# Optimization experiments

Hardware: AMD Instinct MI355X
Metric: run time of the kernel (lower is better)

## Reference

```python
import jax, jax.numpy as jnp
import numpy as np

N, IN_DIM, H_DIM, POS_DIM, K, M, E, OUT_DIM = 50000, 256, 96, 32, 64, 128, 800000, 40
HID = H_DIM + POS_DIM  # 128

def _lin(key, fan_out, fan_in):
    k1, k2 = jax.random.split(key)
    bnd = 1.0 / np.sqrt(fan_in)
    W = jax.random.uniform(k1, (fan_out, fan_in), minval=-bnd, maxval=bnd, dtype=jnp.float32)
    b = jax.random.uniform(k2, (fan_out,), minval=-bnd, maxval=bnd, dtype=jnp.float32)
    return W, b

def setup_inputs() -> dict:
    key = jax.random.key(0)
    ks = jax.random.split(key, 12)
    x = jax.random.normal(ks[0], (N, IN_DIM), dtype=jnp.float32)
    eigenvectors = jax.random.normal(ks[1], (N, M), dtype=jnp.float32)
    eigenvalues = jax.random.uniform(ks[2], (M,), dtype=jnp.float32)
    edge_index = jax.random.randint(ks[3], (2, E), 0, N, dtype=jnp.int64)
    W_feat, b_feat = _lin(ks[4], H_DIM, IN_DIM)
    alpha = jax.random.uniform(ks[5], (K, POS_DIM), minval=-1/np.sqrt(K), maxval=1/np.sqrt(K), dtype=jnp.float32)
    Wl1, bl1 = _lin(ks[6], HID, HID)
    Wr1, _ = _lin(ks[7], HID, HID)
    Wl2, bl2 = _lin(ks[8], HID, HID)
    Wr2, _ = _lin(ks[9], HID, HID)
    W_ro, b_ro = _lin(ks[10], OUT_DIM, HID)
    return dict(x=x, eigenvectors=eigenvectors, eigenvalues=eigenvalues, edge_index=edge_index,
                W_feat=W_feat, b_feat=b_feat, alpha=alpha,
                Wl1=Wl1, bl1=bl1, Wr1=Wr1, Wl2=Wl2, bl2=bl2, Wr2=Wr2,
                W_ro=W_ro, b_ro=b_ro)

def _sage_conv(x, src, dst, Wl, bl, Wr):
    # PyG SAGEConv (mean aggr): out = lin_l(mean_{j->i} x_j) + lin_r(x_i)
    n = x.shape[0]
    agg = jax.ops.segment_sum(x[src], dst, num_segments=n)           # [N, HID]
    cnt = jax.ops.segment_sum(jnp.ones_like(dst, dtype=x.dtype), dst, num_segments=n)
    mean = agg / jnp.maximum(cnt, 1.0)[:, None]
    return mean @ Wl.T + bl + x @ Wr.T

def reference(x, eigenvectors, eigenvalues, edge_index,
              W_feat, b_feat, alpha, Wl1, bl1, Wr1, Wl2, bl2, Wr2, W_ro, b_ro):
    # normalize eigenvectors per column to [-1, 1]
    ev_min = jnp.min(eigenvectors, axis=0, keepdims=True)
    ev_max = jnp.max(eigenvectors, axis=0, keepdims=True)
    ev = (eigenvectors - ev_min) / (ev_max - ev_min) * 2.0 - 1.0
    # normalize eigenvalues to [-1, 1], Chebyshev basis via arccos/cos
    lmin, lmax = jnp.min(eigenvalues), jnp.max(eigenvalues)
    lam = (eigenvalues - lmin) / (lmax - lmin) * 2.0 - 1.0
    theta = jnp.arccos(lam)[:, None] * jnp.arange(K, dtype=lam.dtype)[None, :]  # [M, K]
    pe = jnp.cos(theta) @ alpha                                                  # [M, pos_dim]
    pos = ev @ pe                                                                # [N, pos_dim]
    h = jnp.concatenate([x @ W_feat.T + b_feat, pos], axis=-1)                   # [N, HID]
    src, dst = edge_index[0], edge_index[1]
    h = jax.nn.relu(_sage_conv(h, src, dst, Wl1, bl1, Wr1))
    h = jax.nn.relu(_sage_conv(h, src, dst, Wl2, bl2, Wr2))
    out = jax.nn.log_softmax(h @ W_ro.T + b_ro, axis=-1)
    return out, pe
```

## Files before the change

### kernel.cpp

```cpp
#include <hip/hip_runtime.h>
#include <math.h>

#define N        50000
#define IN_DIM   256
#define H_DIM    96
#define POS_DIM  32
#define KCH      64
#define M        128
#define NE       800000
#define OUT_DIM  40
#define HID      128
#define NSCAN    196
#define NTILES   ((N + 63) / 64)
#define NBK      391
#define BKCAP    2560
#define NSCATB   512
#define SREG     1563

typedef __attribute__((ext_vector_type(8))) short short8v;
typedef __attribute__((ext_vector_type(4))) float float4v;

__device__ __forceinline__ unsigned short f2bf(float f){
  unsigned u = __float_as_uint(f);
  u += 0x7fffu + ((u >> 16) & 1u);
  return (unsigned short)(u >> 16);
}
__device__ __forceinline__ float bf_lo(unsigned u){ return __uint_as_float(u << 16); }
__device__ __forceinline__ float bf_hi(unsigned u){ return __uint_as_float(u & 0xffff0000u); }

__device__ __forceinline__ unsigned enc_key(float f){
  unsigned u = __float_as_uint(f);
  return (u & 0x80000000u) ? ~u : (u | 0x80000000u);
}
__device__ __forceinline__ float dec_key(unsigned k){
  unsigned u = (k & 0x80000000u) ? (k ^ 0x80000000u) : ~k;
  return __uint_as_float(u);
}

__global__ void k_init(unsigned* __restrict__ encmn, unsigned* __restrict__ encmx,
                       short* __restrict__ WT_pos, float* __restrict__ bias_pos,
                       int* __restrict__ bkt_cnt){
  int i = blockIdx.x*blockDim.x + threadIdx.x;
  if (i < M){ encmn[i] = 0xFFFFFFFFu; encmx[i] = 0u; bias_pos[i] = 0.f; }
  if (i < M*M) WT_pos[i] = 0;
  if (i < NBK) bkt_cnt[i] = 0;
}

__global__ __launch_bounds__(256) void k_colminmax(const float* __restrict__ ev,
    unsigned* __restrict__ encmn, unsigned* __restrict__ encmx){
  __shared__ float4 smn[256], smx[256];
  int tid = threadIdx.x;
  int cg  = tid & 31;
  int rs  = blockIdx.x*8 + (tid >> 5);
  int stride = gridDim.x*8;
  float4 mn = make_float4( 3.4e38f,  3.4e38f,  3.4e38f,  3.4e38f);
  float4 mx = make_float4(-3.4e38f, -3.4e38f, -3.4e38f, -3.4e38f);
  #pragma unroll 4
  for (int r = rs; r < N; r += stride){
    float4 v = *(const float4*)&ev[(size_t)r*M + cg*4];
    mn.x = fminf(mn.x, v.x); mn.y = fminf(mn.y, v.y);
    mn.z = fminf(mn.z, v.z); mn.w = fminf(mn.w, v.w);
    mx.x = fmaxf(mx.x, v.x); mx.y = fmaxf(mx.y, v.y);
    mx.z = fmaxf(mx.z, v.z); mx.w = fmaxf(mx.w, v.w);
  }
  smn[tid] = mn; smx[tid] = mx;
  __syncthreads();
  for (int s = 128; s >= 32; s >>= 1){
    if (tid < s){
      float4 a = smn[tid], b = smn[tid + s];
      smn[tid] = make_float4(fminf(a.x,b.x), fminf(a.y,b.y), fminf(a.z,b.z), fminf(a.w,b.w));
      float4 c = smx[tid], d = smx[tid + s];
      smx[tid] = make_float4(fmaxf(c.x,d.x), fmaxf(c.y,d.y), fmaxf(c.z,d.z), fmaxf(c.w,d.w));
    }
    __syncthreads();
  }
  if (tid < 32){
    float4 a = smn[tid], b = smx[tid];
    atomicMin(&encmn[tid*4+0], enc_key(a.x));
    atomicMin(&encmn[tid*4+1], enc_key(a.y));
    atomicMin(&encmn[tid*4+2], enc_key(a.z));
    atomicMin(&encmn[tid*4+3], enc_key(a.w));
    atomicMax(&encmx[tid*4+0], enc_key(b.x));
    atomicMax(&encmx[tid*4+1], enc_key(b.y));
    atomicMax(&encmx[tid*4+2], enc_key(b.z));
    atomicMax(&encmx[tid*4+3], enc_key(b.w));
  }
}

__global__ __launch_bounds__(128) void k_eig_minmax(const float* __restrict__ eigval,
                                                    float* __restrict__ lmm){
  __shared__ float red[M];
  int t = threadIdx.x;
  float v = eigval[t];
  red[t] = v; __syncthreads();
  for (int s = 64; s; s >>= 1){ if (t < s) red[t] = fminf(red[t], red[t+s]); __syncthreads(); }
  if (t == 0) lmm[0] = red[0];
  __syncthreads();
  red[t] = v; __syncthreads();
  for (int s = 64; s; s >>= 1){ if (t < s) red[t] = fmaxf(red[t], red[t+s]); __syncthreads(); }
  if (t == 0) lmm[1] = red[0];
}

__global__ __launch_bounds__(256) void k_pe(
    const float* __restrict__ eigval, const float* __restrict__ alpha,
    const unsigned* __restrict__ encmn, const unsigned* __restrict__ encmx,
    const float* __restrict__ lmm,
    short* __restrict__ WT_pos, float* __restrict__ pe_raw,
    float* __restrict__ pe_out){
  int g = blockIdx.x*256 + threadIdx.x;
  int m = g >> 5, p = g & 31;
  float lmin = lmm[0], lmax = lmm[1];
  float v = eigval[m];
  float lam = (v - lmin)/(lmax - lmin)*2.0f - 1.0f;
  lam = fminf(1.0f, fmaxf(-1.0f, lam));
  float t0 = 1.0f, t1 = lam;
  float acc = alpha[p] + lam*alpha[POS_DIM + p];
  float two_lam = lam + lam;
  #pragma unroll
  for (int k = 2; k < KCH; ++k){
    float t2 = fmaf(two_lam, t1, -t0);
    acc = fmaf(t2, alpha[k*POS_DIM + p], acc);
    t0 = t1; t1 = t2;
  }
  pe_out[g] = acc;
  pe_raw[g] = acc;
  float cmn = dec_key(encmn[m]);
  float cmx = dec_key(encmx[m]);
  float A = 2.0f/(cmx - cmn);
  WT_pos[p*M + m] = (short)f2bf(A*acc);
}

__global__ __launch_bounds__(256) void k_bias(
    const unsigned* __restrict__ encmn, const unsigned* __restrict__ encmx,
    const float* __restrict__ pe_raw, float* __restrict__ bias_pos){
  __shared__ float s[256];
  int tid = threadIdx.x;
  int p = tid >> 3, c = tid & 7;
  float sum = 0.f;
  for (int m = c*16; m < c*16 + 16; ++m){
    float cmn = dec_key(encmn[m]);
    float cmx = dec_key(encmx[m]);
    float A = 2.0f/(cmx - cmn);
    float B = -cmn*A - 1.0f;
    sum += B*pe_raw[m*POS_DIM + p];
  }
  s[tid] = sum;
  __syncthreads();
  if (c == 0){
    float t = 0.f;
    #pragma unroll
    for (int j = 0; j < 8; ++j) t += s[p*8 + j];
    bias_pos[p] = t;
  }
}

__global__ void k_prep_w(const float* __restrict__ Wf, const float* __restrict__ bfeat,
                         const float* __restrict__ Wl1, const float* __restrict__ Wr1,
                         const float* __restrict__ Wl2, const float* __restrict__ Wr2,
                         const float* __restrict__ Wro, const float* __restrict__ bro,
                         short* __restrict__ WTf, float* __restrict__ biasf,
                         short* __restrict__ Wc1, short* __restrict__ Wc2,
                         short* __restrict__ WTro, float* __restrict__ biasro){
  int i = blockIdx.x*256 + threadIdx.x;
  if (i < 128*256){
    int c = i >> 8, k = i & 255;
    WTf[i] = (c < H_DIM) ? (short)f2bf(Wf[c*IN_DIM + k]) : (short)0;
    Wc1[i] = (short)f2bf((k < HID) ? Wl1[c*HID + k] : Wr1[c*HID + k - HID]);
    Wc2[i] = (short)f2bf((k < HID) ? Wl2[c*HID + k] : Wr2[c*HID + k - HID]);
  }
  if (i < 48*128){
    int c = i >> 7, k = i & 127;
    WTro[i] = (c < OUT_DIM) ? (short)f2bf(Wro[c*HID + k]) : (short)0;
  }
  if (i < 128) biasf[i] = (i < H_DIM) ? bfeat[i] : 0.f;
  if (i >= 128 && i < 176) biasro[i - 128] = (i - 128 < OUT_DIM) ? bro[i - 128] : 0.f;
}

template<int KD, bool TWOSRC, bool RELU>
__global__ __launch_bounds__(256) void k_gemm(
    const void* __restrict__ A0v, const void* __restrict__ A1v,
    const short* __restrict__ WT, const float* __restrict__ bias,
    unsigned short* __restrict__ outp, int c_used)
{
  constexpr int KSTEPS = KD/32;
  constexpr int CHR    = KD/8;
  __shared__ short a_lds[64*KD];

  int tid = threadIdx.x;
  int wid = tid >> 6, lane = tid & 63;
  int colBase = wid*32;
  int lrow = lane & 15, lk = (lane >> 4)*8;

  short8v bfrag[KSTEPS][2];
  #pragma unroll
  for (int s = 0; s < KSTEPS; ++s)
    #pragma unroll
    for (int ct = 0; ct < 2; ++ct){
      int col = colBase + ct*16 + lrow;
      bfrag[s][ct] = *(const short8v*)&WT[col*KD + s*32 + lk];
    }
  float b0 = bias[colBase + lrow], b1 = bias[colBase + 16 + lrow];

  for (int tile = blockIdx.x; tile < NTILES; tile += gridDim.x){
    int n0 = tile*64;
    __syncthreads();
    #pragma unroll
    for (int c = tid; c < 64*CHR; c += 256){
      int row = c / CHR;
      int k8  = c % CHR;
      int gn  = min(n0 + row, N-1);
      short8v vv;
      if constexpr (TWOSRC){
        const short* src = (k8 < 16) ? ((const short*)A0v + (size_t)gn*HID + k8*8)
                                     : ((const short*)A1v + (size_t)gn*HID + (k8-16)*8);
        vv = *(const short8v*)src;
      } else {
        const float* src = (const float*)A0v + (size_t)gn*KD + k8*8;
        float4v f0 = *(const float4v*)src;
        float4v f1 = *(const float4v*)(src + 4);
        vv[0] = (short)f2bf(f0[0]); vv[1] = (short)f2bf(f0[1]);
        vv[2] = (short)f2bf(f0[2]); vv[3] = (short)f2bf(f0[3]);
        vv[4] = (short)f2bf(f1[0]); vv[5] = (short)f2bf(f1[1]);
        vv[6] = (short)f2bf(f1[2]); vv[7] = (short)f2bf(f1[3]);
      }
      unsigned off = (unsigned)(row*(KD*2) + k8*16);
      off ^= (unsigned)((row & 7) << 4);
      *(short8v*)((char*)a_lds + off) = vv;
    }
    __syncthreads();
    float4v acc[4][2];
    #pragma unroll
    for (int nt = 0; nt < 4; ++nt){
      acc[nt][0] = (float4v){0.f,0.f,0.f,0.f};
      acc[nt][1] = (float4v){0.f,0.f,0.f,0.f};
    }
    #pragma unroll
    for (int s = 0; s < KSTEPS; ++s){
      #pragma unroll
      for (int nt = 0; nt < 4; ++nt){
        int row = nt*16 + lrow;
        unsigned off = (unsigned)(row*(KD*2) + (s*32 + lk)*2);
        off ^= (unsigned)((row & 7) << 4);
        short8v a = *(const short8v*)((const char*)a_lds + off);
        acc[nt][0] = __builtin_amdgcn_mfma_f32_16x16x32_bf16(a, bfrag[s][0], acc[nt][0], 0, 0, 0);
        acc[nt][1] = __builtin_amdgcn_mfma_f32_16x16x32_bf16(a, bfrag[s][1], acc[nt][1], 0, 0, 0);
      }
    }
    if (colBase < c_used){
      int rbase = (lane >> 4)*4;
      #pragma unroll
      for (int nt = 0; nt < 4; ++nt){
        #pragma unroll
        for (int ct = 0; ct < 2; ++ct){
          int col = colBase + ct*16 + lrow;
          float bb = ct ? b1 : b0;
          #pragma unroll
          for (int r = 0; r < 4; ++r){
            int node = n0 + nt*16 + rbase + r;
            if (node < N){
              float v = acc[nt][ct][r] + bb;
              if (RELU) v = fmaxf(v, 0.f);
              outp[(size_t)node*HID + col] = f2bf(v);
            }
          }
        }
      }
    }
  }
}

__global__ __launch_bounds__(256) void k_hist(const int* __restrict__ dst,
                                              int* __restrict__ bkt_cnt){
  __shared__ int h[NBK];
  int tid = threadIdx.x;
  for (int i = tid; i < NBK; i += 256) h[i] = 0;
  __syncthreads();
  for (int e = blockIdx.x*256 + tid; e < NE; e += gridDim.x*256)
    atomicAdd(&h[dst[e] >> 7], 1);
  __syncthreads();
  for (int i = tid; i < NBK; i += 256){
    int c = h[i];
    if (c) atomicAdd(&bkt_cnt[i], c);
  }
}

__global__ __launch_bounds__(512) void k_bktscan(const int* __restrict__ bkt_cnt,
    int* __restrict__ bkt_start, int* __restrict__ bkt_cursor){
  __shared__ int s[512];
  int t = threadIdx.x;
  int v = (t < NBK) ? bkt_cnt[t] : 0;
  s[t] = v;
  __syncthreads();
  for (int st = 1; st < 512; st <<= 1){
    int a = (t >= st) ? s[t-st] : 0;
    __syncthreads();
    s[t] += a;
    __syncthreads();
  }
  int excl = s[t] - v;
  if (t < NBK){ bkt_start[t] = excl; bkt_cursor[t] = excl; }
  if (t == 0) bkt_start[NBK] = NE;
}

__global__ __launch_bounds__(256) void k_bscatter(const int* __restrict__ src,
    const int* __restrict__ dst, int* __restrict__ bkt_cursor,
    unsigned* __restrict__ estage){
  __shared__ int lcnt[NBK];
  __shared__ int lbase[NBK];
  int tid = threadIdx.x;
  int e0 = blockIdx.x*SREG;
  int e1 = min(e0 + SREG, NE);
  for (int i = tid; i < NBK; i += 256) lcnt[i] = 0;
  __syncthreads();
  for (int e = e0 + tid; e < e1; e += 256)
    atomicAdd(&lcnt[dst[e] >> 7], 1);
  __syncthreads();
  for (int i = tid; i < NBK; i += 256){
    int c = lcnt[i];
    lbase[i] = c ? atomicAdd(&bkt_cursor[i], c) : 0;
    lcnt[i] = 0;
  }
  __syncthreads();
  for (int e = e0 + tid; e < e1; e += 256){
    int d = dst[e];
    int b = d >> 7;
    int slot = lbase[b] + atomicAdd(&lcnt[b], 1);
    estage[slot] = (unsigned)src[e] | ((unsigned)(d & 127) << 16);
  }
}

__global__ __launch_bounds__(256) void k_bcsr(const int* __restrict__ bkt_start,
    const unsigned* __restrict__ estage, unsigned short* __restrict__ csr,
    int* __restrict__ row_ptr){
  __shared__ unsigned eb[BKCAP];
  __shared__ int ncnt[128], sc[128], noff[128];
  int tid = threadIdx.x;
  int b = blockIdx.x;
  int s = bkt_start[b], e = bkt_start[b+1];
  int cnt = min(e - s, BKCAP);
  for (int i = tid; i < cnt; i += 256) eb[i] = estage[s + i];
  if (tid < 128) ncnt[tid] = 0;
  __syncthreads();
  for (int i = tid; i < cnt; i += 256)
    atomicAdd(&ncnt[(eb[i] >> 16) & 127], 1);
  __syncthreads();
  if (tid < 128) sc[tid] = ncnt[tid];
  __syncthreads();
  for (int st = 1; st < 128; st <<= 1){
    int a = (tid < 128 && tid >= st) ? sc[tid-st] : 0;
    __syncthreads();
    if (tid < 128) sc[tid] += a;
    __syncthreads();
  }
  if (tid < 128){
    int excl = sc[tid] - ncnt[tid];
    noff[tid] = excl;
    int node = b*128 + tid;
    if (node <= N) row_ptr[node] = s + excl;
    ncnt[tid] = 0;
  }
  __syncthreads();
  for (int i = tid; i < cnt; i += 256){
    unsigned v = eb[i];
    int ld = (v >> 16) & 127;
    int slot = noff[ld] + atomicAdd(&ncnt[ld], 1);
    csr[s + slot] = (unsigned short)(v & 0xffffu);
  }
}

__global__ __launch_bounds__(256) void k_agg_b(const unsigned* __restrict__ h,
    const int* __restrict__ row_ptr, const unsigned short* __restrict__ csr,
    unsigned* __restrict__ outm){
  int gid = blockIdx.x*blockDim.x + threadIdx.x;
  int i = gid >> 6;
  int lane = gid & 63;
  if (i >= N) return;
  int grp = lane >> 4;
  int lc  = lane & 15;
  int b = row_ptr[i], e = row_ptr[i+1];
  float a[8] = {0.f,0.f,0.f,0.f,0.f,0.f,0.f,0.f};
  for (int j = b + grp; j < e; j += 4){
    int s = csr[j];
    uint4 v = *(const uint4*)&h[(size_t)s*64 + lc*4];
    a[0] += bf_lo(v.x); a[1] += bf_hi(v.x);
    a[2] += bf_lo(v.y); a[3] += bf_hi(v.y);
    a[4] += bf_lo(v.z); a[5] += bf_hi(v.z);
    a[6] += bf_lo(v.w); a[7] += bf_hi(v.w);
  }
  #pragma unroll
  for (int k = 0; k < 8; ++k){
    a[k] += __shfl_xor(a[k], 16, 64);
    a[k] += __shfl_xor(a[k], 32, 64);
  }
  if (grp == 0){
    float inv = 1.0f / fmaxf((float)(e - b), 1.0f);
    uint4 o;
    o.x = (unsigned)f2bf(a[0]*inv) | ((unsigned)f2bf(a[1]*inv) << 16);
    o.y = (unsigned)f2bf(a[2]*inv) | ((unsigned)f2bf(a[3]*inv) << 16);
    o.z = (unsigned)f2bf(a[4]*inv) | ((unsigned)f2bf(a[5]*inv) << 16);
    o.w = (unsigned)f2bf(a[6]*inv) | ((unsigned)f2bf(a[7]*inv) << 16);
    *(uint4*)&outm[(size_t)i*64 + lc*4] = o;
  }
}

__global__ __launch_bounds__(256) void k_readout(const short* __restrict__ hb,
    const short* __restrict__ WTro, const float* __restrict__ biasro,
    float* __restrict__ out){
  __shared__ short a_lds[64*HID];
  int tid = threadIdx.x;
  int wid = tid >> 6, lane = tid & 63;
  int lrow = lane & 15, lk = (lane >> 4)*8;

  short8v bfrag[4][3];
  #pragma unroll
  for (int s = 0; s < 4; ++s)
    #pragma unroll
    for (int t = 0; t < 3; ++t){
      int col = t*16 + lrow;
      bfrag[s][t] = *(const short8v*)&WTro[col*HID + s*32 + lk];
    }
  float bias[3] = { biasro[lrow], biasro[16 + lrow], biasro[32 + lrow] };
  bool val2 = lrow < 8;

  for (int tile = blockIdx.x; tile < NTILES; tile += gridDim.x){
    int n0 = tile*64;
    __syncthreads();
    #pragma unroll
    for (int c = tid; c < 64*16; c += 256){
      int row = c >> 4, k8 = c & 15;
      int gn = min(n0 + row, N-1);
      short8v vv = *(const short8v*)(hb + (size_t)gn*HID + k8*8);
      unsigned off = (unsigned)(row*256 + k8*16);
      off ^= (unsigned)((row & 7) << 4);
      *(short8v*)((char*)a_lds + off) = vv;
    }
    __syncthreads();
    float4v acc[3];
    acc[0] = (float4v){0.f,0.f,0.f,0.f};
    acc[1] = (float4v){0.f,0.f,0.f,0.f};
    acc[2] = (float4v){0.f,0.f,0.f,0.f};
    #pragma unroll
    for (int s = 0; s < 4; ++s){
      int row = wid*16 + lrow;
      unsigned off = (unsigned)(row*256 + (s*32 + lk)*2);
      off ^= (unsigned)((row & 7) << 4);
      short8v a = *(const short8v*)((const char*)a_lds + off);
      acc[0] = __builtin_amdgcn_mfma_f32_16x16x32_bf16(a, bfrag[s][0], acc[0], 0, 0, 0);
      acc[1] = __builtin_amdgcn_mfma_f32_16x16x32_bf16(a, bfrag[s][1], acc[1], 0, 0, 0);
      acc[2] = __builtin_amdgcn_mfma_f32_16x16x32_bf16(a, bfrag[s][2], acc[2], 0, 0, 0);
    }
    #pragma unroll
    for (int r = 0; r < 4; ++r){
      float v0 = acc[0][r] + bias[0];
      float v1 = acc[1][r] + bias[1];
      float v2 = acc[2][r] + bias[2];
      float m = fmaxf(v0, v1);
      m = fmaxf(m, val2 ? v2 : -3.4e38f);
      #pragma unroll
      for (int off = 1; off < 16; off <<= 1) m = fmaxf(m, __shfl_xor(m, off, 64));
      float e = expf(v0 - m) + expf(v1 - m) + (val2 ? expf(v2 - m) : 0.f);
      #pragma unroll
      for (int off = 1; off < 16; off <<= 1) e += __shfl_xor(e, off, 64);
      float lz = m + logf(e);
      int node = n0 + wid*16 + (lane >> 4)*4 + r;
      if (node < N){
        out[(size_t)node*OUT_DIM + lrow]      = v0 - lz;
        out[(size_t)node*OUT_DIM + 16 + lrow] = v1 - lz;
        if (val2) out[(size_t)node*OUT_DIM + 32 + lrow] = v2 - lz;
      }
    }
  }
}

extern "C" void kernel_launch(void* const* d_in, const int* in_sizes, int n_in,
                              void* d_out, int out_size, void* d_ws, size_t ws_size,
                              hipStream_t stream){
  const float* x     = (const float*)d_in[0];
  const float* ev    = (const float*)d_in[1];
  const float* eigv  = (const float*)d_in[2];
  const int*   ei    = (const int*)d_in[3];
  const float* Wf    = (const float*)d_in[4];
  const float* bf    = (const float*)d_in[5];
  const float* alpha = (const float*)d_in[6];
  const float* Wl1   = (const float*)d_in[7];
  const float* bl1   = (const float*)d_in[8];
  const float* Wr1   = (const float*)d_in[9];
  const float* Wl2   = (const float*)d_in[10];
  const float* bl2   = (const float*)d_in[11];
  const float* Wr2   = (const float*)d_in[12];
  const float* Wro   = (const float*)d_in[13];
  const float* bro   = (const float*)d_in[14];
  float* out = (float*)d_out;

  short* h0b    = (short*)d_ws;
  short* h1b    = h0b + (size_t)N*HID;
  short* meanb  = h1b + (size_t)N*HID;
  short* WTf    = meanb + (size_t)N*HID;
  short* Wc1    = WTf + 128*256;
  short* Wc2    = Wc1 + 128*256;
  short* WT_pos = Wc2 + 128*256;
  short* WTro   = WT_pos + 128*128;
  float* biasf    = (float*)(WTro + 48*128);
  float* bias_pos = biasf + 128;
  float* biasro   = bias_pos + 128;
  unsigned* encmn = (unsigned*)(biasro + 48);
  unsigned* encmx = encmn + M;
  int* bkt_cnt    = (int*)(encmx + M);
  int* bkt_start  = bkt_cnt + NBK;
  int* bkt_cursor = bkt_start + NBK + 1;
  int* row_ptr    = bkt_cursor + NBK;
  unsigned* estage = (unsigned*)(row_ptr + N + 1);
  unsigned short* csr = (unsigned short*)(estage + NE);
  float* pe_raw = (float*)(csr + NE);
  float* lmm    = pe_raw + M*POS_DIM;

  const int* srcA = ei;
  const int* dstA = ei + NE;

  k_init<<<NSCAN, 256, 0, stream>>>(encmn, encmx, WT_pos, bias_pos, bkt_cnt);
  k_colminmax<<<256, 256, 0, stream>>>(ev, encmn, encmx);
  k_eig_minmax<<<1, 128, 0, stream>>>(eigv, lmm);
  k_pe<<<16, 256, 0, stream>>>(eigv, alpha, encmn, encmx, lmm, WT_pos, pe_raw,
                               out + (size_t)N*OUT_DIM);
  k_bias<<<1, 256, 0, stream>>>(encmn, encmx, pe_raw, bias_pos);
  k_prep_w<<<128, 256, 0, stream>>>(Wf, bf, Wl1, Wr1, Wl2, Wr2, Wro, bro,
                                    WTf, biasf, Wc1, Wc2, WTro, biasro);
  k_hist<<<512, 256, 0, stream>>>(dstA, bkt_cnt);
  k_bktscan<<<1, 512, 0, stream>>>(bkt_cnt, bkt_start, bkt_cursor);
  k_bscatter<<<NSCATB, 256, 0, stream>>>(srcA, dstA, bkt_cursor, estage);
  k_bcsr<<<NBK, 256, 0, stream>>>(bkt_start, estage, csr, row_ptr);
  k_gemm<256,false,false><<<NTILES, 256, 0, stream>>>(x, nullptr, WTf, biasf,
      (unsigned short*)h0b, 128);
  k_gemm<128,false,false><<<NTILES, 256, 0, stream>>>(ev, nullptr, WT_pos, bias_pos,
      (unsigned short*)(h0b + H_DIM), 32);
  k_agg_b<<<(N*64)/256, 256, 0, stream>>>((const unsigned*)h0b, row_ptr, csr, (unsigned*)meanb);
  k_gemm<256,true,true><<<NTILES, 256, 0, stream>>>(meanb, h0b, Wc1, bl1,
      (unsigned short*)h1b, 128);
  k_agg_b<<<(N*64)/256, 256, 0, stream>>>((const unsigned*)h1b, row_ptr, csr, (unsigned*)meanb);
  k_gemm<256,true,true><<<NTILES, 256, 0, stream>>>(meanb, h1b, Wc2, bl2,
      (unsigned short*)h0b, 128);
  k_readout<<<NTILES, 256, 0, stream>>>(h0b, WTro, biasro, out);
}
```

Before: 235.2 us.

## Fuse input GEMMs, conv2 with readout, eig minmax into PE, unroll aggregation

Merges the feature and positional-encoding GEMMs into one kernel that stages x and eigenvectors together in LDS, with the fourth wave handling the positional columns. Fuses the second SAGE conv GEMM with the readout and log-softmax through an LDS buffer, so the intermediate hidden state is never written to or re-read from global memory. Folds the eigenvalue min/max reduction into the PE kernel and unrolls the neighbor aggregation loop by two to keep more loads in flight. This removes three launches and several global round trips, at the cost of a larger LDS footprint (48KB plus 16KB per block) and an imbalanced wave in the input GEMM.

```diff
diff --git a/kernel.cpp b/kernel.cpp
--- a/kernel.cpp
+++ b/kernel.cpp
@@ -87,29 +87,22 @@
   }
 }
 
-__global__ __launch_bounds__(128) void k_eig_minmax(const float* __restrict__ eigval,
-                                                    float* __restrict__ lmm){
-  __shared__ float red[M];
-  int t = threadIdx.x;
-  float v = eigval[t];
-  red[t] = v; __syncthreads();
-  for (int s = 64; s; s >>= 1){ if (t < s) red[t] = fminf(red[t], red[t+s]); __syncthreads(); }
-  if (t == 0) lmm[0] = red[0];
-  __syncthreads();
-  red[t] = v; __syncthreads();
-  for (int s = 64; s; s >>= 1){ if (t < s) red[t] = fmaxf(red[t], red[t+s]); __syncthreads(); }
-  if (t == 0) lmm[1] = red[0];
-}
-
 __global__ __launch_bounds__(256) void k_pe(
     const float* __restrict__ eigval, const float* __restrict__ alpha,
     const unsigned* __restrict__ encmn, const unsigned* __restrict__ encmx,
-    const float* __restrict__ lmm,
     short* __restrict__ WT_pos, float* __restrict__ pe_raw,
     float* __restrict__ pe_out){
-  int g = blockIdx.x*256 + threadIdx.x;
+  __shared__ float rmn[128], rmx[128];
+  int tid = threadIdx.x;
+  if (tid < 128){ float v = eigval[tid]; rmn[tid] = v; rmx[tid] = v; }
+  __syncthreads();
+  for (int s = 64; s; s >>= 1){
+    if (tid < s){ rmn[tid] = fminf(rmn[tid], rmn[tid+s]); rmx[tid] = fmaxf(rmx[tid], rmx[tid+s]); }
+    __syncthreads();
+  }
+  float lmin = rmn[0], lmax = rmx[0];
+  int g = blockIdx.x*256 + tid;
   int m = g >> 5, p = g & 31;
-  float lmin = lmm[0], lmax = lmm[1];
   float v = eigval[m];
   float lam = (v - lmin)/(lmax - lmin)*2.0f - 1.0f;
   lam = fminf(1.0f, fmaxf(-1.0f, lam));
@@ -176,28 +169,125 @@
   if (i >= 128 && i < 176) biasro[i - 128] = (i - 128 < OUT_DIM) ? bro[i - 128] : 0.f;
 }
 
-template<int KD, bool TWOSRC, bool RELU>
-__global__ __launch_bounds__(256) void k_gemm(
-    const void* __restrict__ A0v, const void* __restrict__ A1v,
+__global__ __launch_bounds__(256) void k_gemm_in(
+    const float* __restrict__ x, const float* __restrict__ ev,
+    const short* __restrict__ WTf, const float* __restrict__ biasf,
+    const short* __restrict__ WT_pos, const float* __restrict__ bias_pos,
+    unsigned short* __restrict__ outp)
+{
+  __shared__ short a_lds[64*384];
+  int tid = threadIdx.x;
+  int wid = tid >> 6, lane = tid & 63;
+  int lrow = lane & 15, lk = (lane >> 4)*8;
+  bool isPos = (wid == 3);
+
+  short8v bfragF[8][2];
+  short8v bfragP[4][2];
+  float b0, b1;
+  if (!isPos){
+    int colBase = wid*32;
+    #pragma unroll
+    for (int s = 0; s < 8; ++s)
+      #pragma unroll
+      for (int ct = 0; ct < 2; ++ct){
+        int col = colBase + ct*16 + lrow;
+        bfragF[s][ct] = *(const short8v*)&WTf[col*256 + s*32 + lk];
+      }
+    b0 = biasf[colBase + lrow]; b1 = biasf[colBase + 16 + lrow];
+  } else {
+    #pragma unroll
+    for (int s = 0; s < 4; ++s)
+      #pragma unroll
+      for (int ct = 0; ct < 2; ++ct){
+        int col = ct*16 + lrow;
+        bfragP[s][ct] = *(const short8v*)&WT_pos[col*128 + s*32 + lk];
+      }
+    b0 = bias_pos[lrow]; b1 = bias_pos[16 + lrow];
+  }
+
+  for (int tile = blockIdx.x; tile < NTILES; tile += gridDim.x){
+    int n0 = tile*64;
+    __syncthreads();
+    for (int c = tid; c < 64*48; c += 256){
+      int row = c / 48, k8 = c % 48;
+      int gn = min(n0 + row, N-1);
+      const float* src = (k8 < 32) ? &x[(size_t)gn*IN_DIM + k8*8]
+                                   : &ev[(size_t)gn*M + (k8-32)*8];
+      float4v f0 = *(const float4v*)src;
+      float4v f1 = *(const float4v*)(src + 4);
+      short8v vv;
+      vv[0] = (short)f2bf(f0[0]); vv[1] = (short)f2bf(f0[1]);
+      vv[2] = (short)f2bf(f0[2]); vv[3] = (short)f2bf(f0[3]);
+      vv[4] = (short)f2bf(f1[0]); vv[5] = (short)f2bf(f1[1]);
+      vv[6] = (short)f2bf(f1[2]); vv[7] = (short)f2bf(f1[3]);
+      unsigned off = (unsigned)(row*768 + k8*16) ^ (unsigned)((row & 7) << 4);
+      *(short8v*)((char*)a_lds + off) = vv;
+    }
+    __syncthreads();
+    float4v acc[4][2];
+    #pragma unroll
+    for (int nt = 0; nt < 4; ++nt){
+      acc[nt][0] = (float4v){0.f,0.f,0.f,0.f};
+      acc[nt][1] = (float4v){0.f,0.f,0.f,0.f};
+    }
+    if (!isPos){
+      #pragma unroll
+      for (int s = 0; s < 8; ++s)
+        #pragma unroll
+        for (int nt = 0; nt < 4; ++nt){
+          int row = nt*16 + lrow;
+          unsigned off = (unsigned)(row*768 + (s*32 + lk)*2) ^ (unsigned)((row & 7) << 4);
+          short8v a = *(const short8v*)((const char*)a_lds + off);
+          acc[nt][0] = __builtin_amdgcn_mfma_f32_16x16x32_bf16(a, bfragF[s][0], acc[nt][0], 0, 0, 0);
+          acc[nt][1] = __builtin_amdgcn_mfma_f32_16x16x32_bf16(a, bfragF[s][1], acc[nt][1], 0, 0, 0);
+        }
+    } else {
+      #pragma unroll
+      for (int s = 0; s < 4; ++s)
+        #pragma unroll
+        for (int nt = 0; nt < 4; ++nt){
+          int row = nt*16 + lrow;
+          unsigned off = (unsigned)(row*768 + 512 + (s*32 + lk)*2) ^ (unsigned)((row & 7) << 4);
+          short8v a = *(const short8v*)((const char*)a_lds + off);
+          acc[nt][0] = __builtin_amdgcn_mfma_f32_16x16x32_bf16(a, bfragP[s][0], acc[nt][0], 0, 0, 0);
+          acc[nt][1] = __builtin_amdgcn_mfma_f32_16x16x32_bf16(a, bfragP[s][1], acc[nt][1], 0, 0, 0);
+        }
+    }
+    int colBase = isPos ? 96 : wid*32;
+    int rbase = (lane >> 4)*4;
+    #pragma unroll
+    for (int nt = 0; nt < 4; ++nt)
+      #pragma unroll
+      for (int ct = 0; ct < 2; ++ct){
+        int col = colBase + ct*16 + lrow;
+        float bb = ct ? b1 : b0;
+        #pragma unroll
+        for (int r = 0; r < 4; ++r){
+          int node = n0 + nt*16 + rbase + r;
+          if (node < N) outp[(size_t)node*HID + col] = f2bf(acc[nt][ct][r] + bb);
+        }
+      }
+  }
+}
+
+__global__ __launch_bounds__(256) void k_conv(
+    const short* __restrict__ A0, const short* __restrict__ A1,
     const short* __restrict__ WT, const float* __restrict__ bias,
-    unsigned short* __restrict__ outp, int c_used)
+    unsigned short* __restrict__ outp)
 {
-  constexpr int KSTEPS = KD/32;
-  constexpr int CHR    = KD/8;
-  __shared__ short a_lds[64*KD];
-
+  __shared__ short a_lds[64*256];
   int tid = threadIdx.x;
   int wid = tid >> 6, lane = tid & 63;
   int colBase = wid*32;
   int lrow = lane & 15, lk = (lane >> 4)*8;
 
-  short8v bfrag[KSTEPS][2];
+  short8v bfrag[8][2];
   #pragma unroll
-  for (int s = 0; s < KSTEPS; ++s)
+  for (int s = 0; s < 8; ++s)
     #pragma unroll
     for (int ct = 0; ct < 2; ++ct){
       int col = colBase + ct*16 + lrow;
-      bfrag[s][ct] = *(const short8v*)&WT[col*KD + s*32 + lk];
+      bfrag[s][ct] = *(const short8v*)&WT[col*256 + s*32 + lk];
     }
   float b0 = bias[colBase + lrow], b1 = bias[colBase + 16 + lrow];
 
@@ -205,26 +295,13 @@
     int n0 = tile*64;
     __syncthreads();
     #pragma unroll
-    for (int c = tid; c < 64*CHR; c += 256){
-      int row = c / CHR;
-      int k8  = c % CHR;
-      int gn  = min(n0 + row, N-1);
-      short8v vv;
-      if constexpr (TWOSRC){
-        const short* src = (k8 < 16) ? ((const short*)A0v + (size_t)gn*HID + k8*8)
-                                     : ((const short*)A1v + (size_t)gn*HID + (k8-16)*8);
-        vv = *(const short8v*)src;
-      } else {
-        const float* src = (const float*)A0v + (size_t)gn*KD + k8*8;
-        float4v f0 = *(const float4v*)src;
-        float4v f1 = *(const float4v*)(src + 4);
-        vv[0] = (short)f2bf(f0[0]); vv[1] = (short)f2bf(f0[1]);
-        vv[2] = (short)f2bf(f0[2]); vv[3] = (short)f2bf(f0[3]);
-        vv[4] = (short)f2bf(f1[0]); vv[5] = (short)f2bf(f1[1]);
-        vv[6] = (short)f2bf(f1[2]); vv[7] = (short)f2bf(f1[3]);
-      }
-      unsigned off = (unsigned)(row*(KD*2) + k8*16);
-      off ^= (unsigned)((row & 7) << 4);
+    for (int c = tid; c < 64*32; c += 256){
+      int row = c >> 5, k8 = c & 31;
+      int gn = min(n0 + row, N-1);
+      const short* src = (k8 < 16) ? (A0 + (size_t)gn*HID + k8*8)
+                                   : (A1 + (size_t)gn*HID + (k8-16)*8);
+      short8v vv = *(const short8v*)src;
+      unsigned off = (unsigned)(row*512 + k8*16) ^ (unsigned)((row & 7) << 4);
       *(short8v*)((char*)a_lds + off) = vv;
     }
     __syncthreads();
@@ -235,35 +312,143 @@
       acc[nt][1] = (float4v){0.f,0.f,0.f,0.f};
     }
     #pragma unroll
-    for (int s = 0; s < KSTEPS; ++s){
+    for (int s = 0; s < 8; ++s)
       #pragma unroll
       for (int nt = 0; nt < 4; ++nt){
         int row = nt*16 + lrow;
-        unsigned off = (unsigned)(row*(KD*2) + (s*32 + lk)*2);
-        off ^= (unsigned)((row & 7) << 4);
+        unsigned off = (unsigned)(row*512 + (s*32 + lk)*2) ^ (unsigned)((row & 7) << 4);
         short8v a = *(const short8v*)((const char*)a_lds + off);
         acc[nt][0] = __builtin_amdgcn_mfma_f32_16x16x32_bf16(a, bfrag[s][0], acc[nt][0], 0, 0, 0);
         acc[nt][1] = __builtin_amdgcn_mfma_f32_16x16x32_bf16(a, bfrag[s][1], acc[nt][1], 0, 0, 0);
       }
-    }
-    if (colBase < c_used){
-      int rbase = (lane >> 4)*4;
+    int rbase = (lane >> 4)*4;
+    #pragma unroll
+    for (int nt = 0; nt < 4; ++nt)
+      #pragma unroll
+      for (int ct = 0; ct < 2; ++ct){
+        int col = colBase + ct*16 + lrow;
+        float bb = ct ? b1 : b0;
+        #pragma unroll
+        for (int r = 0; r < 4; ++r){
+          int node = n0 + nt*16 + rbase + r;
+          if (node < N)
+            outp[(size_t)node*HID + col] = f2bf(fmaxf(acc[nt][ct][r] + bb, 0.f));
+        }
+      }
+  }
+}
+
+__global__ __launch_bounds__(256) void k_conv_ro(
+    const short* __restrict__ A0, const short* __restrict__ A1,
+    const short* __restrict__ WT, const float* __restrict__ bias,
+    const short* __restrict__ WTro, const float* __restrict__ biasro,
+    float* __restrict__ out)
+{
+  __shared__ short a_lds[64*256];
+  __shared__ short o_lds[64*128];
+  int tid = threadIdx.x;
+  int wid = tid >> 6, lane = tid & 63;
+  int colBase = wid*32;
+  int lrow = lane & 15, lk = (lane >> 4)*8;
+
+  short8v bfrag[8][2];
+  #pragma unroll
+  for (int s = 0; s < 8; ++s)
+    #pragma unroll
+    for (int ct = 0; ct < 2; ++ct){
+      int col = colBase + ct*16 + lrow;
+      bfrag[s][ct] = *(const short8v*)&WT[col*256 + s*32 + lk];
+    }
+  float b0 = bias[colBase + lrow], b1 = bias[colBase + 16 + lrow];
+
+  short8v bfragR[4][3];
+  #pragma unroll
+  for (int s = 0; s < 4; ++s)
+    #pragma unroll
+    for (int t = 0; t < 3; ++t){
+      int col = t*16 + lrow;
+      bfragR[s][t] = *(const short8v*)&WTro[col*HID + s*32 + lk];
+    }
+  float biasR[3] = { biasro[lrow], biasro[16 + lrow], biasro[32 + lrow] };
+  bool val2 = lrow < 8;
+
+  for (int tile = blockIdx.x; tile < NTILES; tile += gridDim.x){
+    int n0 = tile*64;
+    __syncthreads();
+    #pragma unroll
+    for (int c = tid; c < 64*32; c += 256){
+      int row = c >> 5, k8 = c & 31;
+      int gn = min(n0 + row, N-1);
+      const short* src = (k8 < 16) ? (A0 + (size_t)gn*HID + k8*8)
+                                   : (A1 + (size_t)gn*HID + (k8-16)*8);
+      short8v vv = *(const short8v*)src;
+      unsigned off = (unsigned)(row*512 + k8*16) ^ (unsigned)((row & 7) << 4);
+      *(short8v*)((char*)a_lds + off) = vv;
+    }
+    __syncthreads();
+    float4v acc[4][2];
+    #pragma unroll
+    for (int nt = 0; nt < 4; ++nt){
+      acc[nt][0] = (float4v){0.f,0.f,0.f,0.f};
+      acc[nt][1] = (float4v){0.f,0.f,0.f,0.f};
+    }
+    #pragma unroll
+    for (int s = 0; s < 8; ++s)
       #pragma unroll
       for (int nt = 0; nt < 4; ++nt){
+        int row = nt*16 + lrow;
+        unsigned off = (unsigned)(row*512 + (s*32 + lk)*2) ^ (unsigned)((row & 7) << 4);
+        short8v a = *(const short8v*)((const char*)a_lds + off);
+        acc[nt][0] = __builtin_amdgcn_mfma_f32_16x16x32_bf16(a, bfrag[s][0], acc[nt][0], 0, 0, 0);
+        acc[nt][1] = __builtin_amdgcn_mfma_f32_16x16x32_bf16(a, bfrag[s][1], acc[nt][1], 0, 0, 0);
+      }
+    int rbase = (lane >> 4)*4;
+    #pragma unroll
+    for (int nt = 0; nt < 4; ++nt)
+      #pragma unroll
+      for (int ct = 0; ct < 2; ++ct){
+        int col = colBase + ct*16 + lrow;
+        float bb = ct ? b1 : b0;
         #pragma unroll
-        for (int ct = 0; ct < 2; ++ct){
-          int col = colBase + ct*16 + lrow;
-          float bb = ct ? b1 : b0;
-          #pragma unroll
-          for (int r = 0; r < 4; ++r){
-            int node = n0 + nt*16 + rbase + r;
-            if (node < N){
-              float v = acc[nt][ct][r] + bb;
-              if (RELU) v = fmaxf(v, 0.f);
-              outp[(size_t)node*HID + col] = f2bf(v);
-            }
-          }
+        for (int r = 0; r < 4; ++r){
+          int row = nt*16 + rbase + r;
+          float v = fmaxf(acc[nt][ct][r] + bb, 0.f);
+          unsigned off = (unsigned)(row*256 + col*2) ^ (unsigned)((row & 7) << 4);
+          *(short*)((char*)o_lds + off) = (short)f2bf(v);
         }
+      }
+    __syncthreads();
+    float4v acc3[3];
+    acc3[0] = (float4v){0.f,0.f,0.f,0.f};
+    acc3[1] = (float4v){0.f,0.f,0.f,0.f};
+    acc3[2] = (float4v){0.f,0.f,0.f,0.f};
+    #pragma unroll
+    for (int s = 0; s < 4; ++s){
+      int row = wid*16 + lrow;
+      unsigned off = (unsigned)(row*256 + (s*32 + lk)*2) ^ (unsigned)((row & 7) << 4);
+      short8v a = *(const short8v*)((const char*)o_lds + off);
+      acc3[0] = __builtin_amdgcn_mfma_f32_16x16x32_bf16(a, bfragR[s][0], acc3[0], 0, 0, 0);
+      acc3[1] = __builtin_amdgcn_mfma_f32_16x16x32_bf16(a, bfragR[s][1], acc3[1], 0, 0, 0);
+      acc3[2] = __builtin_amdgcn_mfma_f32_16x16x32_bf16(a, bfragR[s][2], acc3[2], 0, 0, 0);
+    }
+    #pragma unroll
+    for (int r = 0; r < 4; ++r){
+      float v0 = acc3[0][r] + biasR[0];
+      float v1 = acc3[1][r] + biasR[1];
+      float v2 = acc3[2][r] + biasR[2];
+      float mx = fmaxf(v0, v1);
+      mx = fmaxf(mx, val2 ? v2 : -3.4e38f);
+      #pragma unroll
+      for (int off = 1; off < 16; off <<= 1) mx = fmaxf(mx, __shfl_xor(mx, off, 64));
+      float e = expf(v0 - mx) + expf(v1 - mx) + (val2 ? expf(v2 - mx) : 0.f);
+      #pragma unroll
+      for (int off = 1; off < 16; off <<= 1) e += __shfl_xor(e, off, 64);
+      float lz = mx + logf(e);
+      int node = n0 + wid*16 + (lane >> 4)*4 + r;
+      if (node < N){
+        out[(size_t)node*OUT_DIM + lrow]      = v0 - lz;
+        out[(size_t)node*OUT_DIM + 16 + lrow] = v1 - lz;
+        if (val2) out[(size_t)node*OUT_DIM + 32 + lrow] = v2 - lz;
       }
     }
   }
@@ -378,97 +563,46 @@
   int grp = lane >> 4;
   int lc  = lane & 15;
   int b = row_ptr[i], e = row_ptr[i+1];
-  float a[8] = {0.f,0.f,0.f,0.f,0.f,0.f,0.f,0.f};
-  for (int j = b + grp; j < e; j += 4){
-    int s = csr[j];
-    uint4 v = *(const uint4*)&h[(size_t)s*64 + lc*4];
-    a[0] += bf_lo(v.x); a[1] += bf_hi(v.x);
-    a[2] += bf_lo(v.y); a[3] += bf_hi(v.y);
-    a[4] += bf_lo(v.z); a[5] += bf_hi(v.z);
-    a[6] += bf_lo(v.w); a[7] += bf_hi(v.w);
+  float a0[8] = {0.f,0.f,0.f,0.f,0.f,0.f,0.f,0.f};
+  float a1[8] = {0.f,0.f,0.f,0.f,0.f,0.f,0.f,0.f};
+  int j = b + grp;
+  for (; j + 4 < e; j += 8){
+    int s0 = csr[j];
+    int s1 = csr[j+4];
+    uint4 v0 = *(const uint4*)&h[(size_t)s0*64 + lc*4];
+    uint4 v1 = *(const uint4*)&h[(size_t)s1*64 + lc*4];
+    a0[0] += bf_lo(v0.x); a0[1] += bf_hi(v0.x);
+    a0[2] += bf_lo(v0.y); a0[3] += bf_hi(v0.y);
+    a0[4] += bf_lo(v0.z); a0[5] += bf_hi(v0.z);
+    a0[6] += bf_lo(v0.w); a0[7] += bf_hi(v0.w);
+    a1[0] += bf_lo(v1.x); a1[1] += bf_hi(v1.x);
+    a1[2] += bf_lo(v1.y); a1[3] += bf_hi(v1.y);
+    a1[4] += bf_lo(v1.z); a1[5] += bf_hi(v1.z);
+    a1[6] += bf_lo(v1.w); a1[7] += bf_hi(v1.w);
+  }
+  if (j < e){
+    int s0 = csr[j];
+    uint4 v0 = *(const uint4*)&h[(size_t)s0*64 + lc*4];
+    a0[0] += bf_lo(v0.x); a0[1] += bf_hi(v0.x);
+    a0[2] += bf_lo(v0.y); a0[3] += bf_hi(v0.y);
+    a0[4] += bf_lo(v0.z); a0[5] += bf_hi(v0.z);
+    a0[6] += bf_lo(v0.w); a0[7] += bf_hi(v0.w);
   }
   #pragma unroll
   for (int k = 0; k < 8; ++k){
-    a[k] += __shfl_xor(a[k], 16, 64);
-    a[k] += __shfl_xor(a[k], 32, 64);
+    float t = a0[k] + a1[k];
+    t += __shfl_xor(t, 16, 64);
+    t += __shfl_xor(t, 32, 64);
+    a0[k] = t;
   }
   if (grp == 0){
     float inv = 1.0f / fmaxf((float)(e - b), 1.0f);
     uint4 o;
-    o.x = (unsigned)f2bf(a[0]*inv) | ((unsigned)f2bf(a[1]*inv) << 16);
-    o.y = (unsigned)f2bf(a[2]*inv) | ((unsigned)f2bf(a[3]*inv) << 16);
-    o.z = (unsigned)f2bf(a[4]*inv) | ((unsigned)f2bf(a[5]*inv) << 16);
-    o.w = (unsigned)f2bf(a[6]*inv) | ((unsigned)f2bf(a[7]*inv) << 16);
+    o.x = (unsigned)f2bf(a0[0]*inv) | ((unsigned)f2bf(a0[1]*inv) << 16);
+    o.y = (unsigned)f2bf(a0[2]*inv) | ((unsigned)f2bf(a0[3]*inv) << 16);
+    o.z = (unsigned)f2bf(a0[4]*inv) | ((unsigned)f2bf(a0[5]*inv) << 16);
+    o.w = (unsigned)f2bf(a0[6]*inv) | ((unsigned)f2bf(a0[7]*inv) << 16);
     *(uint4*)&outm[(size_t)i*64 + lc*4] = o;
-  }
-}
-
-__global__ __launch_bounds__(256) void k_readout(const short* __restrict__ hb,
-    const short* __restrict__ WTro, const float* __restrict__ biasro,
-    float* __restrict__ out){
-  __shared__ short a_lds[64*HID];
-  int tid = threadIdx.x;
-  int wid = tid >> 6, lane = tid & 63;
-  int lrow = lane & 15, lk = (lane >> 4)*8;
-
-  short8v bfrag[4][3];
-  #pragma unroll
-  for (int s = 0; s < 4; ++s)
-    #pragma unroll
-    for (int t = 0; t < 3; ++t){
-      int col = t*16 + lrow;
-      bfrag[s][t] = *(const short8v*)&WTro[col*HID + s*32 + lk];
-    }
-  float bias[3] = { biasro[lrow], biasro[16 + lrow], biasro[32 + lrow] };
-  bool val2 = lrow < 8;
-
-  for (int tile = blockIdx.x; tile < NTILES; tile += gridDim.x){
-    int n0 = tile*64;
-    __syncthreads();
-    #pragma unroll
-    for (int c = tid; c < 64*16; c += 256){
-      int row = c >> 4, k8 = c & 15;
-      int gn = min(n0 + row, N-1);
-      short8v vv = *(const short8v*)(hb + (size_t)gn*HID + k8*8);
-      unsigned off = (unsigned)(row*256 + k8*16);
-      off ^= (unsigned)((row & 7) << 4);
-      *(short8v*)((char*)a_lds + off) = vv;
-    }
-    __syncthreads();
-    float4v acc[3];
-    acc[0] = (float4v){0.f,0.f,0.f,0.f};
-    acc[1] = (float4v){0.f,0.f,0.f,0.f};
-    acc[2] = (float4v){0.f,0.f,0.f,0.f};
-    #pragma unroll
-    for (int s = 0; s < 4; ++s){
-      int row = wid*16 + lrow;
-      unsigned off = (unsigned)(row*256 + (s*32 + lk)*2);
-      off ^= (unsigned)((row & 7) << 4);
-      short8v a = *(const short8v*)((const char*)a_lds + off);
-      acc[0] = __builtin_amdgcn_mfma_f32_16x16x32_bf16(a, bfrag[s][0], acc[0], 0, 0, 0);
-      acc[1] = __builtin_amdgcn_mfma_f32_16x16x32_bf16(a, bfrag[s][1], acc[1], 0, 0, 0);
-      acc[2] = __builtin_amdgcn_mfma_f32_16x16x32_bf16(a, bfrag[s][2], acc[2], 0, 0, 0);
-    }
-    #pragma unroll
-    for (int r = 0; r < 4; ++r){
-      float v0 = acc[0][r] + bias[0];
-      float v1 = acc[1][r] + bias[1];
-      float v2 = acc[2][r] + bias[2];
-      float m = fmaxf(v0, v1);
-      m = fmaxf(m, val2 ? v2 : -3.4e38f);
-      #pragma unroll
-      for (int off = 1; off < 16; off <<= 1) m = fmaxf(m, __shfl_xor(m, off, 64));
-      float e = expf(v0 - m) + expf(v1 - m) + (val2 ? expf(v2 - m) : 0.f);
-      #pragma unroll
-      for (int off = 1; off < 16; off <<= 1) e += __shfl_xor(e, off, 64);
-      float lz = m + logf(e);
-      int node = n0 + wid*16 + (lane >> 4)*4 + r;
-      if (node < N){
-        out[(size_t)node*OUT_DIM + lrow]      = v0 - lz;
-        out[(size_t)node*OUT_DIM + 16 + lrow] = v1 - lz;
-        if (val2) out[(size_t)node*OUT_DIM + 32 + lrow] = v2 - lz;
-      }
-    }
   }
 }
 
@@ -512,15 +646,13 @@
   unsigned* estage = (unsigned*)(row_ptr + N + 1);
   unsigned short* csr = (unsigned short*)(estage + NE);
   float* pe_raw = (float*)(csr + NE);
-  float* lmm    = pe_raw + M*POS_DIM;
 
   const int* srcA = ei;
   const int* dstA = ei + NE;
 
   k_init<<<NSCAN, 256, 0, stream>>>(encmn, encmx, WT_pos, bias_pos, bkt_cnt);
   k_colminmax<<<256, 256, 0, stream>>>(ev, encmn, encmx);
-  k_eig_minmax<<<1, 128, 0, stream>>>(eigv, lmm);
-  k_pe<<<16, 256, 0, stream>>>(eigv, alpha, encmn, encmx, lmm, WT_pos, pe_raw,
+  k_pe<<<16, 256, 0, stream>>>(eigv, alpha, encmn, encmx, WT_pos, pe_raw,
                                out + (size_t)N*OUT_DIM);
   k_bias<<<1, 256, 0, stream>>>(encmn, encmx, pe_raw, bias_pos);
   k_prep_w<<<128, 256, 0, stream>>>(Wf, bf, Wl1, Wr1, Wl2, Wr2, Wro, bro,
@@ -529,15 +661,10 @@
   k_bktscan<<<1, 512, 0, stream>>>(bkt_cnt, bkt_start, bkt_cursor);
   k_bscatter<<<NSCATB, 256, 0, stream>>>(srcA, dstA, bkt_cursor, estage);
   k_bcsr<<<NBK, 256, 0, stream>>>(bkt_start, estage, csr, row_ptr);
-  k_gemm<256,false,false><<<NTILES, 256, 0, stream>>>(x, nullptr, WTf, biasf,
-      (unsigned short*)h0b, 128);
-  k_gemm<128,false,false><<<NTILES, 256, 0, stream>>>(ev, nullptr, WT_pos, bias_pos,
-      (unsigned short*)(h0b + H_DIM), 32);
+  k_gemm_in<<<NTILES, 256, 0, stream>>>(x, ev, WTf, biasf, WT_pos, bias_pos,
+                                        (unsigned short*)h0b);
   k_agg_b<<<(N*64)/256, 256, 0, stream>>>((const unsigned*)h0b, row_ptr, csr, (unsigned*)meanb);
-  k_gemm<256,true,true><<<NTILES, 256, 0, stream>>>(meanb, h0b, Wc1, bl1,
-      (unsigned short*)h1b, 128);
+  k_conv<<<NTILES, 256, 0, stream>>>(meanb, h0b, Wc1, bl1, (unsigned short*)h1b);
   k_agg_b<<<(N*64)/256, 256, 0, stream>>>((const unsigned*)h1b, row_ptr, csr, (unsigned*)meanb);
-  k_gemm<256,true,true><<<NTILES, 256, 0, stream>>>(meanb, h1b, Wc2, bl2,
-      (unsigned short*)h0b, 128);
-  k_readout<<<NTILES, 256, 0, stream>>>(h0b, WTro, biasro, out);
-}
+  k_conv_ro<<<NTILES, 256, 0, stream>>>(meanb, h1b, Wc2, bl2, WTro, biasro, out);
+}
```

After: 225.4 us. -4.2%, faster.
